# Kernel tuning notes

Hardware: AMD Instinct MI355X
Metric: run time of the kernel (lower is better)

## Reference

```python
import jax, jax.numpy as jnp
import numpy as np

B, S, HID, H, DH = 8, 4096, 1024, 16, 64


def setup_inputs() -> dict:
    key = jax.random.key(0)
    ks = jax.random.split(key, 5)
    return {
        "hidden_states": jax.random.normal(ks[0], (B, S, HID), dtype=jnp.float32),
        "attention_mask": jnp.ones((B, 1, 1, S), dtype=jnp.float32),
        "Wq": jax.random.normal(ks[1], (HID, HID), dtype=jnp.float32) * (HID ** -0.5),
        "Wk": jax.random.normal(ks[2], (HID, HID), dtype=jnp.float32) * (HID ** -0.5),
        "Wv": jax.random.normal(ks[3], (HID, HID), dtype=jnp.float32) * (HID ** -0.5),
        "att_weight": jax.random.normal(ks[4], (H, 1, DH), dtype=jnp.float32) * (DH ** -0.5),
    }


def _heads(x):
    # [B,S,HID] -> [B,H,S,DH]
    b, s, _ = x.shape
    return x.reshape(b, s, H, DH).transpose(0, 2, 1, 3)


def reference(hidden_states, attention_mask, Wq, Wk, Wv, att_weight):
    # bias-free projections (torch Linear: x @ W.T)
    q = _heads(hidden_states @ Wq.T)  # [B,H,S,DH]
    k = _heads(hidden_states @ Wk.T)
    v = _heads(hidden_states @ Wv.T)

    mask = attention_mask.transpose(0, 1, 3, 2)  # [B,1,S,1]
    aw = att_weight[:, 0, :]  # [H,DH]

    q_scores = jnp.einsum('bhsd,hd->bhs', q, aw)[..., None] * mask  # [B,H,S,1]
    k_scores = jnp.einsum('bhsd,hd->bhs', k, aw)[..., None] * mask  # [B,H,S,1]

    length = jnp.sum(mask, axis=-2, keepdims=True)            # [B,1,1,1]
    mean_value = jnp.sum(v * mask, axis=-2, keepdims=True)    # [B,H,1,DH]

    query_values = q_scores * mean_value                      # [B,H,S,DH] outer product
    key_values = jnp.einsum('bhs,bhsd->bhd', k_scores[..., 0], v)[:, :, None, :]  # [B,H,1,DH]

    ctx = (query_values + key_values) / length                # [B,H,S,DH]
    ctx = ctx.transpose(0, 2, 1, 3).reshape(ctx.shape[0], ctx.shape[2], H * DH)
    return ctx
```

## Files before the change

kernel.cpp:

```cpp
#include <hip/hip_runtime.h>

#define BB 8
#define SS 4096
#define HIDD 1024
#define HH 16
#define DHH 64

__global__ __launch_bounds__(256) void k_prep(const float* __restrict__ Wq,
                                              const float* __restrict__ Wk,
                                              const float* __restrict__ aw,
                                              float* __restrict__ wq_f,
                                              float* __restrict__ wk_f) {
    int i = blockIdx.x * 256 + threadIdx.x;
    int h = blockIdx.y;
    const float* W = blockIdx.z ? Wk : Wq;
    float* outp = blockIdx.z ? wk_f : wq_f;
    float acc = 0.f;
#pragma unroll
    for (int d = 0; d < DHH; ++d) {
        acc += aw[h * DHH + d] * W[(size_t)(h * DHH + d) * HIDD + i];
    }
    outp[h * HIDD + i] = acc;
}

#define KC 64
#define NCH (HIDD / KC)
__global__ __launch_bounds__(512) void k_scores(const float* __restrict__ hid,
                                                const float* __restrict__ mask,
                                                const float* __restrict__ weff,
                                                float* __restrict__ qsb,
                                                float* __restrict__ ksb) {
    __shared__ float shh[2][64 * KC];
    __shared__ float shw[2][32 * KC];

    const int t    = threadIdx.x;
    const int lane = t & 63;
    const int wave = t >> 6;
    const int obase = __builtin_amdgcn_readfirstlane(wave * 4);

    const int row  = blockIdx.x * 64 + lane;
    const size_t gbase = (size_t)blockIdx.x * 64 * HIDD;
    const int swz = lane & 7;

    float acc[4] = {0.f, 0.f, 0.f, 0.f};

    auto stage = [&](int chunk, int buf) {
#pragma unroll
        for (int j = 0; j < 2; ++j) {
            int f  = j * 512 + t;
            int r  = f >> 4;
            int cp = f & 15;
            int c  = cp ^ (r & 7);
            const float* gp = hid + gbase + (size_t)r * HIDD + chunk * KC + c * 4;
            float* lp = &shh[buf][f * 4];
            __builtin_amdgcn_global_load_lds(
                (const __attribute__((address_space(1))) void*)gp,
                (__attribute__((address_space(3))) void*)lp, 16, 0, 0);
        }
        {
            int o  = t >> 4;
            int cp = t & 15;
            const float* gp = weff + (size_t)o * HIDD + chunk * KC + cp * 4;
            float* lp = &shw[buf][t * 4];
            __builtin_amdgcn_global_load_lds(
                (const __attribute__((address_space(1))) void*)gp,
                (__attribute__((address_space(3))) void*)lp, 16, 0, 0);
        }
    };

    stage(0, 0);

    for (int chunk = 0; chunk < NCH; ++chunk) {
        const int buf = chunk & 1;
        asm volatile("s_waitcnt vmcnt(0)" ::: "memory");
        __syncthreads();
        if (chunk + 1 < NCH) stage(chunk + 1, buf ^ 1);

        const float* hb = &shh[buf][lane * KC];
        const float* wb = &shw[buf][0];
#pragma unroll
        for (int kc = 0; kc < KC / 4; ++kc) {
            float4 h4 = *reinterpret_cast<const float4*>(hb + ((kc ^ swz) << 2));
#pragma unroll
            for (int o = 0; o < 4; ++o) {
                float4 wv = *reinterpret_cast<const float4*>(
                    wb + (obase + o) * KC + (kc << 2));
                acc[o] += h4.x * wv.x + h4.y * wv.y + h4.z * wv.z + h4.w * wv.w;
            }
        }
    }

    float m = mask[row];
#pragma unroll
    for (int o = 0; o < 4; ++o) acc[o] *= m;

    float4 v = make_float4(acc[0], acc[1], acc[2], acc[3]);
    if (obase < 16) {
        *reinterpret_cast<float4*>(qsb + (size_t)row * 16 + obase) = v;
    } else {
        *reinterpret_cast<float4*>(ksb + (size_t)row * 20 + (obase - 16)) = v;
        if (obase == 16) ksb[(size_t)row * 20 + 16] = m;
    }
}

__global__ __launch_bounds__(256) void k_ksh(const float* __restrict__ hid,
                                             const float* __restrict__ ksb,
                                             float* __restrict__ part) {
    int b  = blockIdx.y;
    int i  = threadIdx.x * 4;
    int s0 = blockIdx.x * 64;

    float4 acc[17];
#pragma unroll
    for (int c = 0; c < 17; ++c) acc[c] = make_float4(0.f, 0.f, 0.f, 0.f);

    const float* hb = hid + (size_t)(b * SS + s0) * HIDD + i;
    const float* sb = ksb + (size_t)(b * SS + s0) * 20;

#pragma unroll 4
    for (int s = 0; s < 64; ++s) {
        float4 hv = *reinterpret_cast<const float4*>(hb + (size_t)s * HIDD);
        const float* sc = sb + s * 20;
#pragma unroll
        for (int c = 0; c < 17; ++c) {
            float scv = sc[c];
            acc[c].x += scv * hv.x;
            acc[c].y += scv * hv.y;
            acc[c].z += scv * hv.z;
            acc[c].w += scv * hv.w;
        }
    }

    float* pb = part + (((size_t)blockIdx.x * 8 + b) * 17) * 1024 + i;
#pragma unroll
    for (int c = 0; c < 17; ++c) {
        *reinterpret_cast<float4*>(pb + c * 1024) = acc[c];
    }
}

__global__ __launch_bounds__(256) void k_red(const float* __restrict__ part,
                                             float* __restrict__ ksh,
                                             float* __restrict__ hsum) {
    int gid = blockIdx.x * 256 + threadIdx.x;
    int b = gid / 17408;
    int r = gid - b * 17408;
    int c = r >> 10;
    int i = r & 1023;

    float s = 0.f;
#pragma unroll 8
    for (int k = 0; k < 64; ++k)
        s += part[(((size_t)k * 8 + b) * 17 + c) * 1024 + i];

    if (c < 16) ksh[((size_t)b * 16 + c) * 1024 + i] = s;
    else        hsum[b * 1024 + i] = s;
}

__global__ __launch_bounds__(256) void k_fin(const float* __restrict__ Wv,
                                             const float* __restrict__ mask,
                                             const float* __restrict__ hsum,
                                             const float* __restrict__ ksh,
                                             float* __restrict__ mvn,
                                             float* __restrict__ kvn) {
    int b  = blockIdx.x;
    int j  = blockIdx.y * 32 + (threadIdx.x >> 3);
    int sl = threadIdx.x & 7;

    __shared__ float red[256];
    float lsum = 0.f;
    for (int s = threadIdx.x; s < SS; s += 256) lsum += mask[b * SS + s];
    red[threadIdx.x] = lsum;
    __syncthreads();
    for (int off = 128; off; off >>= 1) {
        if (threadIdx.x < off) red[threadIdx.x] += red[threadIdx.x + off];
        __syncthreads();
    }
    float invlen = 1.0f / red[0];

    int h = j >> 6;
    const float4* w4 = reinterpret_cast<const float4*>(Wv + (size_t)j * HIDD + sl * 128);
    const float4* hv = reinterpret_cast<const float4*>(hsum + b * HIDD + sl * 128);
    const float4* kv = reinterpret_cast<const float4*>(ksh + ((size_t)b * 16 + h) * HIDD + sl * 128);

    float mv = 0.f, kvv = 0.f;
#pragma unroll
    for (int c = 0; c < 32; ++c) {
        float4 w = w4[c], a = hv[c], k2 = kv[c];
        mv  += w.x * a.x  + w.y * a.y  + w.z * a.z  + w.w * a.w;
        kvv += w.x * k2.x + w.y * k2.y + w.z * k2.z + w.w * k2.w;
    }
#pragma unroll
    for (int off = 1; off < 8; off <<= 1) {
        mv  += __shfl_xor(mv, off);
        kvv += __shfl_xor(kvv, off);
    }
    if (sl == 0) {
        mvn[b * HIDD + j] = mv * invlen;
        kvn[b * HIDD + j] = kvv * invlen;
    }
}

__global__ __launch_bounds__(256) void k_out(const float* __restrict__ qsb,
                                             const float* __restrict__ mvn,
                                             const float* __restrict__ kvn,
                                             float* __restrict__ outp) {
    size_t e0 = ((size_t)blockIdx.x * 256 + threadIdx.x) * 8;
    int b   = (int)(e0 >> 22);
    int rem = (int)(e0 & ((1u << 22) - 1));
    int s   = rem >> 10;
    int j   = rem & 1023;

    float q = qsb[(size_t)(b * SS + s) * 16 + (j >> 6)];
    const float4* mv4 = reinterpret_cast<const float4*>(mvn + b * HIDD + j);
    const float4* kv4 = reinterpret_cast<const float4*>(kvn + b * HIDD + j);
    float4 m0 = mv4[0], m1 = mv4[1];
    float4 k0 = kv4[0], k1 = kv4[1];

    float4 o0, o1;
    o0.x = q * m0.x + k0.x;  o0.y = q * m0.y + k0.y;
    o0.z = q * m0.z + k0.z;  o0.w = q * m0.w + k0.w;
    o1.x = q * m1.x + k1.x;  o1.y = q * m1.y + k1.y;
    o1.z = q * m1.z + k1.z;  o1.w = q * m1.w + k1.w;

    float4* op = reinterpret_cast<float4*>(outp + e0);
    op[0] = o0;
    op[1] = o1;
}

extern "C" void kernel_launch(void* const* d_in, const int* in_sizes, int n_in,
                              void* d_out, int out_size, void* d_ws, size_t ws_size,
                              hipStream_t stream) {
    const float* hid  = (const float*)d_in[0];
    const float* mask = (const float*)d_in[1];
    const float* Wq   = (const float*)d_in[2];
    const float* Wk   = (const float*)d_in[3];
    const float* Wv   = (const float*)d_in[4];
    const float* aw   = (const float*)d_in[5];
    float* outp = (float*)d_out;

    float* ws   = (float*)d_ws;
    float* wq_f = ws;
    float* wk_f = wq_f + 16384;
    float* qsb  = wk_f + 16384;
    float* ksb  = qsb + 524288;
    float* ksh  = ksb + 655360;
    float* hsum = ksh + 131072;
    float* mvn  = hsum + 8192;
    float* kvn  = mvn + 8192;
    float* part = kvn + 8192;

    k_prep  <<<dim3(4, 16, 2), 256, 0, stream>>>(Wq, Wk, aw, wq_f, wk_f);
    k_scores<<<dim3(512),      512, 0, stream>>>(hid, mask, wq_f, qsb, ksb);
    k_ksh   <<<dim3(64, 8),    256, 0, stream>>>(hid, ksb, part);
    k_red   <<<dim3(544),      256, 0, stream>>>(part, ksh, hsum);
    k_fin   <<<dim3(8, 32),    256, 0, stream>>>(Wv, mask, hsum, ksh, mvn, kvn);
    k_out   <<<dim3(16384),    256, 0, stream>>>(qsb, mvn, kvn, outp);
}
```

Baseline: 343.4 us.

## Process two rows per thread in k_scores with padded LDS layout

Each k_scores block now handles 128 rows instead of 64, so every thread accumulates two rows and reuses each loaded weight float4 for both. The XOR-swizzled LDS layout for hidden states is replaced by a padded stride of 68 floats (17 float4s) to avoid bank conflicts, with an extra staging load for the first 128 threads. The grid halves to 256 blocks, which cuts redundant weight loads from LDS but gives fewer blocks to spread over the CUs and uses more shared memory per block.

```diff
diff --git a/kernel.cpp b/kernel.cpp
--- a/kernel.cpp
+++ b/kernel.cpp
@@ -30,43 +30,59 @@
                                                 const float* __restrict__ weff,
                                                 float* __restrict__ qsb,
                                                 float* __restrict__ ksb) {
-    __shared__ float shh[2][64 * KC];
-    __shared__ float shw[2][32 * KC];
+    __shared__ float shh[2][128 * 17 * 4];
+    __shared__ float shw[2][32 * 16 * 4];
 
     const int t    = threadIdx.x;
     const int lane = t & 63;
     const int wave = t >> 6;
     const int obase = __builtin_amdgcn_readfirstlane(wave * 4);
 
-    const int row  = blockIdx.x * 64 + lane;
-    const size_t gbase = (size_t)blockIdx.x * 64 * HIDD;
-    const int swz = lane & 7;
-
-    float acc[4] = {0.f, 0.f, 0.f, 0.f};
+    const int row0 = blockIdx.x * 128 + lane;
+    const int row1 = row0 + 64;
+    const size_t gbase = (size_t)blockIdx.x * 128 * HIDD;
+
+    int srow[5], scol[5];
+#pragma unroll
+    for (int j = 0; j < 5; ++j) {
+        int f = (j < 4) ? (j * 512 + t) : (2048 + t);
+        int r = f / 17;
+        int c = f - r * 17;
+        srow[j] = r;
+        scol[j] = (c == 16) ? 0 : c;
+    }
+    const bool extra = (t < 128);
 
     auto stage = [&](int chunk, int buf) {
 #pragma unroll
-        for (int j = 0; j < 2; ++j) {
-            int f  = j * 512 + t;
-            int r  = f >> 4;
-            int cp = f & 15;
-            int c  = cp ^ (r & 7);
-            const float* gp = hid + gbase + (size_t)r * HIDD + chunk * KC + c * 4;
-            float* lp = &shh[buf][f * 4];
+        for (int j = 0; j < 4; ++j) {
+            const float* gp = hid + gbase + (size_t)srow[j] * HIDD
+                              + chunk * KC + scol[j] * 4;
+            float* lp = &shh[buf][(j * 512 + t) * 4];
             __builtin_amdgcn_global_load_lds(
                 (const __attribute__((address_space(1))) void*)gp,
                 (__attribute__((address_space(3))) void*)lp, 16, 0, 0);
         }
+        if (extra) {
+            const float* gp = hid + gbase + (size_t)srow[4] * HIDD
+                              + chunk * KC + scol[4] * 4;
+            float* lp = &shh[buf][(2048 + t) * 4];
+            __builtin_amdgcn_global_load_lds(
+                (const __attribute__((address_space(1))) void*)gp,
+                (__attribute__((address_space(3))) void*)lp, 16, 0, 0);
+        }
         {
-            int o  = t >> 4;
-            int cp = t & 15;
-            const float* gp = weff + (size_t)o * HIDD + chunk * KC + cp * 4;
+            const float* gp = weff + (size_t)(t >> 4) * HIDD
+                              + chunk * KC + (t & 15) * 4;
             float* lp = &shw[buf][t * 4];
             __builtin_amdgcn_global_load_lds(
                 (const __attribute__((address_space(1))) void*)gp,
                 (__attribute__((address_space(3))) void*)lp, 16, 0, 0);
         }
     };
+
+    float acc0[4] = {0.f, 0.f, 0.f, 0.f};
+    float acc1[4] = {0.f, 0.f, 0.f, 0.f};
 
     stage(0, 0);
 
@@ -76,30 +92,39 @@
         __syncthreads();
         if (chunk + 1 < NCH) stage(chunk + 1, buf ^ 1);
 
-        const float* hb = &shh[buf][lane * KC];
-        const float* wb = &shw[buf][0];
-#pragma unroll
-        for (int kc = 0; kc < KC / 4; ++kc) {
-            float4 h4 = *reinterpret_cast<const float4*>(hb + ((kc ^ swz) << 2));
+        const float* h0 = &shh[buf][lane * 68];
+        const float* h1 = &shh[buf][(lane + 64) * 68];
+        const float* wb = &shw[buf][obase * 64];
+#pragma unroll
+        for (int kc = 0; kc < 16; ++kc) {
+            float4 a0 = *reinterpret_cast<const float4*>(h0 + kc * 4);
+            float4 a1 = *reinterpret_cast<const float4*>(h1 + kc * 4);
 #pragma unroll
             for (int o = 0; o < 4; ++o) {
-                float4 wv = *reinterpret_cast<const float4*>(
-                    wb + (obase + o) * KC + (kc << 2));
-                acc[o] += h4.x * wv.x + h4.y * wv.y + h4.z * wv.z + h4.w * wv.w;
+                float4 wv = *reinterpret_cast<const float4*>(wb + o * 64 + kc * 4);
+                acc0[o] += a0.x * wv.x + a0.y * wv.y + a0.z * wv.z + a0.w * wv.w;
+                acc1[o] += a1.x * wv.x + a1.y * wv.y + a1.z * wv.z + a1.w * wv.w;
             }
         }
     }
 
-    float m = mask[row];
-#pragma unroll
-    for (int o = 0; o < 4; ++o) acc[o] *= m;
-
-    float4 v = make_float4(acc[0], acc[1], acc[2], acc[3]);
+    float m0 = mask[row0];
+    float m1 = mask[row1];
+#pragma unroll
+    for (int o = 0; o < 4; ++o) { acc0[o] *= m0; acc1[o] *= m1; }
+
+    float4 v0 = make_float4(acc0[0], acc0[1], acc0[2], acc0[3]);
+    float4 v1 = make_float4(acc1[0], acc1[1], acc1[2], acc1[3]);
     if (obase < 16) {
-        *reinterpret_cast<float4*>(qsb + (size_t)row * 16 + obase) = v;
+        *reinterpret_cast<float4*>(qsb + (size_t)row0 * 16 + obase) = v0;
+        *reinterpret_cast<float4*>(qsb + (size_t)row1 * 16 + obase) = v1;
     } else {
-        *reinterpret_cast<float4*>(ksb + (size_t)row * 20 + (obase - 16)) = v;
-        if (obase == 16) ksb[(size_t)row * 20 + 16] = m;
+        *reinterpret_cast<float4*>(ksb + (size_t)row0 * 20 + (obase - 16)) = v0;
+        *reinterpret_cast<float4*>(ksb + (size_t)row1 * 20 + (obase - 16)) = v1;
+        if (obase == 16) {
+            ksb[(size_t)row0 * 20 + 16] = m0;
+            ksb[(size_t)row1 * 20 + 16] = m1;
+        }
     }
 }
 
@@ -250,7 +275,7 @@
     float* part = kvn + 8192;
 
     k_prep  <<<dim3(4, 16, 2), 256, 0, stream>>>(Wq, Wk, aw, wq_f, wk_f);
-    k_scores<<<dim3(512),      512, 0, stream>>>(hid, mask, wq_f, qsb, ksb);
+    k_scores<<<dim3(256),      512, 0, stream>>>(hid, mask, wq_f, qsb, ksb);
     k_ksh   <<<dim3(64, 8),    256, 0, stream>>>(hid, ksb, part);
     k_red   <<<dim3(544),      256, 0, stream>>>(part, ksh, hsum);
     k_fin   <<<dim3(8, 32),    256, 0, stream>>>(Wv, mask, hsum, ksh, mvn, kvn);
```

New measurement: 346.2 us. About the same (+0.8%).
